# Kernel optimization log

Measured on AMD Instinct MI355X. Metric: run time of the kernel, lower is better.

Reference implementation:

```python
import jax, jax.numpy as jnp
import numpy as np


def _dwconv(x, w, pad):
    # depthwise conv, NCHW, weight (C,1,kh,kw), feature_group_count=C
    return jax.lax.conv_general_dilated(
        x, w, window_strides=(1, 1), padding=pad,
        feature_group_count=x.shape[1],
        dimension_numbers=('NCHW', 'OIHW', 'NCHW'))


def _max_channel_relu(x):
    # assumed MaxChannelReLU: keep only the channel-max value at each (b,h,w)
    return x * (x == jnp.max(x, axis=1, keepdims=True))


def setup_inputs() -> dict:
    key = jax.random.key(0)
    ks = jax.random.split(key, 6)
    B, C, H, W = 16, 64, 128, 128
    x = jax.random.normal(ks[0], (B, C, H, W), dtype=jnp.float32)
    w_bbx = 0.1 * jax.random.normal(ks[1], (C, 1, 1, 1), dtype=jnp.float32)
    w_width = 0.1 * jax.random.normal(ks[2], (C, 1, 1, 11), dtype=jnp.float32)
    w_width_sh = 0.1 * jax.random.normal(ks[3], (C, 1, 1, 1), dtype=jnp.float32)
    w_height = 0.1 * jax.random.normal(ks[4], (C, 1, 11, 1), dtype=jnp.float32)
    w_height_sh = 0.1 * jax.random.normal(ks[5], (C, 1, 1, 1), dtype=jnp.float32)
    return {"x": x, "w_bbx": w_bbx, "w_width": w_width,
            "w_width_sh": w_width_sh, "w_height": w_height,
            "w_height_sh": w_height_sh}


def reference(x, w_bbx, w_width, w_width_sh, w_height, w_height_sh):
    B, C, H, W = x.shape
    # self.bbx: depthwise 1x1 conv == per-channel scale
    wh = x * w_bbx.reshape(1, C, 1, 1)
    # width branch: depthwise (1,11) conv pad 5, scaled by W, then shared 1x1
    w = _dwconv(wh, w_width, [(0, 0), (5, 5)]) * W
    w = w * w_width_sh.reshape(1, C, 1, 1)
    # height branch: depthwise (11,1) conv pad 5, scaled by H, then shared 1x1
    h = _dwconv(wh, w_height, [(5, 5), (0, 0)]) * H
    h = h * w_height_sh.reshape(1, C, 1, 1)
    sx = jax.nn.sigmoid(x)
    M = jnp.max(sx, axis=(-2, -1), keepdims=True) - 0.01
    score = x * (sx > M).astype(x.dtype)
    S = jnp.sum(score, axis=(-2, -1), keepdims=True)
    sn = score / S  # normalized weights, reused by all weighted reductions
    ws = jnp.sum(w * sn, axis=(-2, -1))
    hs = jnp.sum(h * sn, axis=(-2, -1))
    ps = jnp.max(sx, axis=(-2, -1))
    col = jnp.arange(W, dtype=x.dtype).reshape(1, 1, 1, W)
    row = jnp.arange(H, dtype=x.dtype).reshape(1, 1, H, 1)
    x1 = jnp.sum(col * sn, axis=(-2, -1)) - ws / 2
    y1 = jnp.sum(row * sn, axis=(-2, -1)) - hs / 2
    x2 = x1 + ws
    y2 = y1 + hs
    score_m = _max_channel_relu(score)
    w_m = _max_channel_relu(w)
    h_m = _max_channel_relu(h)
    i = jnp.broadcast_to(jnp.arange(B, dtype=x.dtype)[:, None], (B, C))
    bbox = jnp.stack([i, x1, y1, x2, y2, ps], axis=-1).reshape(-1, 6)
    return jnp.concatenate([score_m, w_m, h_m], axis=1), bbox
```

## Files before the change

### kernel.cpp

```cpp
#include <hip/hip_runtime.h>
#include <math.h>

#define BATCH 16
#define CH    64
#define HH    128
#define WW    128
#define PLANE (HH*WW)
#define LROW  144
#define LROWS 138
#define OUT0  (BATCH*3*CH*PLANE)


__global__ __launch_bounds__(256) void k_max(const float* __restrict__ x,
                                             float* __restrict__ ws) {
    int bid = blockIdx.x;
    const float4* xp = (const float4*)(x + (size_t)bid * PLANE);
    int tid = threadIdx.x;
    float m = -INFINITY;
#pragma unroll
    for (int i = 0; i < 16; i++) {
        float4 v = xp[i * 256 + tid];
        m = fmaxf(m, fmaxf(fmaxf(v.x, v.y), fmaxf(v.z, v.w)));
    }
#pragma unroll
    for (int off = 32; off; off >>= 1) m = fmaxf(m, __shfl_xor(m, off, 64));
    __shared__ float sm[4];
    int wid = tid >> 6, lane = tid & 63;
    if (lane == 0) sm[wid] = m;
    __syncthreads();
    if (tid == 0) {
        float mm = fmaxf(fmaxf(sm[0], sm[1]), fmaxf(sm[2], sm[3]));
        float ps = 1.0f / (1.0f + expf(-mm));
        ws[bid] = ps - 0.01f;
        ws[1024 + bid] = ps;
    }
}

__global__ __launch_bounds__(256) void k_fields(
    const float* __restrict__ x,
    const float* __restrict__ w_bbx, const float* __restrict__ w_width,
    const float* __restrict__ w_width_sh, const float* __restrict__ w_height,
    const float* __restrict__ w_height_sh,
    float* __restrict__ ws, float* __restrict__ out) {
    __shared__ float xs[LROWS * LROW];
    __shared__ float red[4 * 5];
    int bid = blockIdx.x;
    int b = bid >> 6, c = bid & 63;
    int tid = threadIdx.x;

    for (int i = tid; i < LROWS * LROW; i += 256) xs[i] = 0.0f;
    __syncthreads();
    const float* xp = x + (size_t)bid * PLANE;
#pragma unroll
    for (int i = 0; i < 16; i++) {
        int idx = i * 256 + tid;
        int p = idx * 4;
        int y = p >> 7, xc = p & 127;
        float4 v = ((const float4*)xp)[idx];
        *(float4*)&xs[(y + 5) * LROW + xc + 8] = v;
    }
    float wk[11], hk[11];
#pragma unroll
    for (int k = 0; k < 11; k++) {
        wk[k] = w_width[c * 11 + k];
        hk[k] = w_height[c * 11 + k];
    }
    float cb = w_bbx[c];
    float cw = 128.0f * w_width_sh[c] * cb;
    float chs = 128.0f * w_height_sh[c] * cb;
    float M = ws[bid];
    __syncthreads();

    float S = 0.f, Sw = 0.f, Sh = 0.f, Scol = 0.f, Srow = 0.f;
    float* outS = out + (size_t)(b * 192 + c) * PLANE;
    float* outW = out + (size_t)(b * 192 + 64 + c) * PLANE;
    float* outH = out + (size_t)(b * 192 + 128 + c) * PLANE;

    for (int g = 0; g < 16; g++) {
        int idx = g * 256 + tid;
        int p = idx * 4;
        int y = p >> 7, xc = p & 127;
        float4 vx;
        float hx = 0.f, hy = 0.f, hz = 0.f, hw = 0.f;
#pragma unroll
        for (int k = 0; k < 11; k++) {
            float4 v = *(const float4*)&xs[(y + k) * LROW + xc + 8];
            if (k == 5) vx = v;
            hx += v.x * hk[k]; hy += v.y * hk[k];
            hz += v.z * hk[k]; hw += v.w * hk[k];
        }
        float wbuf[20];
        {
            float4 a0 = *(const float4*)&xs[(y + 5) * LROW + xc + 0];
            float4 a1 = *(const float4*)&xs[(y + 5) * LROW + xc + 4];
            float4 a3 = *(const float4*)&xs[(y + 5) * LROW + xc + 12];
            float4 a4 = *(const float4*)&xs[(y + 5) * LROW + xc + 16];
            wbuf[0] = a0.x;  wbuf[1] = a0.y;  wbuf[2] = a0.z;  wbuf[3] = a0.w;
            wbuf[4] = a1.x;  wbuf[5] = a1.y;  wbuf[6] = a1.z;  wbuf[7] = a1.w;
            wbuf[8] = vx.x;  wbuf[9] = vx.y;  wbuf[10] = vx.z; wbuf[11] = vx.w;
            wbuf[12] = a3.x; wbuf[13] = a3.y; wbuf[14] = a3.z; wbuf[15] = a3.w;
            wbuf[16] = a4.x; wbuf[17] = a4.y; wbuf[18] = a4.z; wbuf[19] = a4.w;
        }
        float wo[4];
#pragma unroll
        for (int j = 0; j < 4; j++) {
            float acc = 0.f;
#pragma unroll
            for (int k = 0; k < 11; k++) acc += wbuf[j + 3 + k] * wk[k];
            wo[j] = acc * cw;
        }
        float ho[4] = {hx * chs, hy * chs, hz * chs, hw * chs};
        float xv[4] = {vx.x, vx.y, vx.z, vx.w};
        float sc[4];
#pragma unroll
        for (int j = 0; j < 4; j++) {
            float sx = 1.0f / (1.0f + expf(-xv[j]));
            sc[j] = (sx > M) ? xv[j] : 0.0f;
        }
        float s4 = sc[0] + sc[1] + sc[2] + sc[3];
        S += s4;
        Srow += (float)y * s4;
#pragma unroll
        for (int j = 0; j < 4; j++) {
            Sw += wo[j] * sc[j];
            Sh += ho[j] * sc[j];
            Scol += (float)(xc + j) * sc[j];
        }
        float4 o;
        o.x = sc[0]; o.y = sc[1]; o.z = sc[2]; o.w = sc[3];
        ((float4*)outS)[idx] = o;
        o.x = wo[0]; o.y = wo[1]; o.z = wo[2]; o.w = wo[3];
        ((float4*)outW)[idx] = o;
        o.x = ho[0]; o.y = ho[1]; o.z = ho[2]; o.w = ho[3];
        ((float4*)outH)[idx] = o;
    }
#pragma unroll
    for (int off = 32; off; off >>= 1) {
        S    += __shfl_xor(S, off, 64);
        Sw   += __shfl_xor(Sw, off, 64);
        Sh   += __shfl_xor(Sh, off, 64);
        Scol += __shfl_xor(Scol, off, 64);
        Srow += __shfl_xor(Srow, off, 64);
    }
    int wid = tid >> 6, lane = tid & 63;
    if (lane == 0) {
        red[wid * 5 + 0] = S;   red[wid * 5 + 1] = Sw;
        red[wid * 5 + 2] = Sh;  red[wid * 5 + 3] = Scol;
        red[wid * 5 + 4] = Srow;
    }
    __syncthreads();
    if (tid == 0) {
        float a0 = 0, a1 = 0, a2 = 0, a3 = 0, a4 = 0;
#pragma unroll
        for (int w2 = 0; w2 < 4; w2++) {
            a0 += red[w2 * 5 + 0]; a1 += red[w2 * 5 + 1];
            a2 += red[w2 * 5 + 2]; a3 += red[w2 * 5 + 3];
            a4 += red[w2 * 5 + 4];
        }
        ws[2048 + bid] = a0;
        ws[3072 + bid] = a1;
        ws[4096 + bid] = a2;
        ws[5120 + bid] = a3;
        ws[6144 + bid] = a4;
    }
}

__global__ __launch_bounds__(256) void k_mask(float* __restrict__ out) {
    __shared__ float T[64 * 256];
    int bid = blockIdx.x;
    int b = bid >> 6;
    int p0 = (bid & 63) * 256;
    int tid = threadIdx.x;
    for (int f = 0; f < 3; f++) {
        size_t base = ((size_t)b * 192 + (size_t)f * 64) * PLANE + p0;
#pragma unroll
        for (int ci = 0; ci < 16; ci++) {
            int ch = ci * 4 + (tid >> 6);
            int px = (tid & 63) * 4;
            float4 v = *(const float4*)&out[base + (size_t)ch * PLANE + px];
            *(float4*)&T[ch * 256 + px] = v;
        }
        __syncthreads();
        float m = -INFINITY;
#pragma unroll
        for (int cc = 0; cc < 64; cc++) m = fmaxf(m, T[cc * 256 + tid]);
#pragma unroll
        for (int cc = 0; cc < 64; cc++) {
            float v = T[cc * 256 + tid];
            T[cc * 256 + tid] = (v == m) ? v : 0.0f;
        }
        __syncthreads();
#pragma unroll
        for (int ci = 0; ci < 16; ci++) {
            int ch = ci * 4 + (tid >> 6);
            int px = (tid & 63) * 4;
            float4 v = *(const float4*)&T[ch * 256 + px];
            *(float4*)&out[base + (size_t)ch * PLANE + px] = v;
        }
        __syncthreads();
    }
}

__global__ __launch_bounds__(256) void k_bbox(const float* __restrict__ ws,
                                              float* __restrict__ out) {
    int idx = blockIdx.x * 256 + threadIdx.x;
    if (idx >= 1024) return;
    int b = idx >> 6;
    float S    = ws[2048 + idx];
    float Sw   = ws[3072 + idx];
    float Sh   = ws[4096 + idx];
    float Scol = ws[5120 + idx];
    float Srow = ws[6144 + idx];
    float ps   = ws[1024 + idx];
    float inv = 1.0f / S;
    float wsv = Sw * inv, hsv = Sh * inv;
    float x1 = Scol * inv - 0.5f * wsv;
    float y1 = Srow * inv - 0.5f * hsv;
    float* o = out + OUT0 + (size_t)idx * 6;
    o[0] = (float)b;
    o[1] = x1;
    o[2] = y1;
    o[3] = x1 + wsv;
    o[4] = y1 + hsv;
    o[5] = ps;
}

extern "C" void kernel_launch(void* const* d_in, const int* in_sizes, int n_in,
                              void* d_out, int out_size, void* d_ws, size_t ws_size,
                              hipStream_t stream) {
    const float* x          = (const float*)d_in[0];
    const float* w_bbx      = (const float*)d_in[1];
    const float* w_width    = (const float*)d_in[2];
    const float* w_width_sh = (const float*)d_in[3];
    const float* w_height   = (const float*)d_in[4];
    const float* w_height_sh= (const float*)d_in[5];
    float* out = (float*)d_out;
    float* ws  = (float*)d_ws;

    k_max<<<dim3(1024), dim3(256), 0, stream>>>(x, ws);
    k_fields<<<dim3(1024), dim3(256), 0, stream>>>(
        x, w_bbx, w_width, w_width_sh, w_height, w_height_sh, ws, out);
    k_mask<<<dim3(1024), dim3(256), 0, stream>>>(out);
    k_bbox<<<dim3(4), dim3(256), 0, stream>>>(ws, out);
}
```

Before: 316.4 us.

## Precompute channel-max maps and fuse max-channel masking into field writer

Adds a pass that recomputes the width/height convolutions and score per pixel across all channels to build channel-max maps. The main kernel then applies the max-channel mask as it writes, eliminating the separate read-modify-write pass over the full output. The sigmoid threshold is also turned into an equivalent logit threshold on x, avoiding exp per element. The cost is redundant convolution compute and extra workspace for the max maps, and the k_cmax grid of only 256 blocks may underfill the GPU.

```diff
diff --git a/kernel.cpp b/kernel.cpp
--- a/kernel.cpp
+++ b/kernel.cpp
@@ -6,12 +6,65 @@
 #define HH    128
 #define WW    128
 #define PLANE (HH*WW)
+#define OUT0  (BATCH*3*CH*PLANE)
+
 #define LROW  144
 #define LROWS 138
-#define OUT0  (BATCH*3*CH*PLANE)
-
+
+#define CW_OFF  7168
+#define CHS_OFF 7232
+#define MW_OFF  8192
+#define MH_OFF  270336
+#define MS_OFF  532480
+
+__device__ __forceinline__ void conv4(const float* __restrict__ base,
+                                      const float* __restrict__ wk,
+                                      const float* __restrict__ hk,
+                                      float cw, float chs, float T,
+                                      float4& w4, float4& h4, float4& s4) {
+    float4 vx;
+    float hx = 0.f, hy = 0.f, hz = 0.f, hw = 0.f;
+#pragma unroll
+    for (int k = 0; k < 11; k++) {
+        float4 v = *(const float4*)(base + k * 144 + 8);
+        if (k == 5) vx = v;
+        hx = fmaf(v.x, hk[k], hx);
+        hy = fmaf(v.y, hk[k], hy);
+        hz = fmaf(v.z, hk[k], hz);
+        hw = fmaf(v.w, hk[k], hw);
+    }
+    float wbuf[20];
+    {
+        float4 a0 = *(const float4*)(base + 5 * 144 + 0);
+        float4 a1 = *(const float4*)(base + 5 * 144 + 4);
+        float4 a3 = *(const float4*)(base + 5 * 144 + 12);
+        float4 a4 = *(const float4*)(base + 5 * 144 + 16);
+        wbuf[0] = a0.x;  wbuf[1] = a0.y;  wbuf[2] = a0.z;  wbuf[3] = a0.w;
+        wbuf[4] = a1.x;  wbuf[5] = a1.y;  wbuf[6] = a1.z;  wbuf[7] = a1.w;
+        wbuf[8] = vx.x;  wbuf[9] = vx.y;  wbuf[10] = vx.z; wbuf[11] = vx.w;
+        wbuf[12] = a3.x; wbuf[13] = a3.y; wbuf[14] = a3.z; wbuf[15] = a3.w;
+        wbuf[16] = a4.x; wbuf[17] = a4.y; wbuf[18] = a4.z; wbuf[19] = a4.w;
+    }
+    float wo[4];
+#pragma unroll
+    for (int j = 0; j < 4; j++) {
+        float acc = 0.f;
+#pragma unroll
+        for (int k = 0; k < 11; k++) acc = fmaf(wbuf[j + 3 + k], wk[k], acc);
+        wo[j] = acc * cw;
+    }
+    w4.x = wo[0]; w4.y = wo[1]; w4.z = wo[2]; w4.w = wo[3];
+    h4.x = hx * chs; h4.y = hy * chs; h4.z = hz * chs; h4.w = hw * chs;
+    s4.x = (vx.x > T) ? vx.x : 0.f;
+    s4.y = (vx.y > T) ? vx.y : 0.f;
+    s4.z = (vx.z > T) ? vx.z : 0.f;
+    s4.w = (vx.w > T) ? vx.w : 0.f;
+}
 
 __global__ __launch_bounds__(256) void k_max(const float* __restrict__ x,
+                                             const float* __restrict__ w_bbx,
+                                             const float* __restrict__ w_width_sh,
+                                             const float* __restrict__ w_height_sh,
                                              float* __restrict__ ws) {
     int bid = blockIdx.x;
     const float4* xp = (const float4*)(x + (size_t)bid * PLANE);
@@ -31,16 +84,84 @@
     if (tid == 0) {
         float mm = fmaxf(fmaxf(sm[0], sm[1]), fmaxf(sm[2], sm[3]));
         float ps = 1.0f / (1.0f + expf(-mm));
-        ws[bid] = ps - 0.01f;
+        float M = ps - 0.01f;
+        float T = (M > 0.0f) ? logf(M / (1.0f - M)) : -INFINITY;
+        ws[bid] = T;
         ws[1024 + bid] = ps;
     }
-}
-
-__global__ __launch_bounds__(256) void k_fields(
+    if (bid < 64 && tid == 1) {
+        float cb = w_bbx[bid];
+        ws[CW_OFF + bid]  = 128.0f * w_width_sh[bid] * cb;
+        ws[CHS_OFF + bid] = 128.0f * w_height_sh[bid] * cb;
+    }
+}
+
+__global__ __launch_bounds__(256) void k_cmax(const float* __restrict__ x,
+                                              const float* __restrict__ w_width,
+                                              const float* __restrict__ w_height,
+                                              float* __restrict__ ws) {
+    __shared__ float4 xs4[4 * 18 * 36];
+    float* xs = (float*)xs4;
+    int bid = blockIdx.x;
+    int b = bid >> 4;
+    int r0 = (bid & 15) * 8;
+    int tid = threadIdx.x;
+
+    for (int i = tid; i < 4 * 18 * 36; i += 256)
+        xs4[i] = make_float4(0.f, 0.f, 0.f, 0.f);
+
+    int lr_o = tid >> 5;
+    int c0 = (tid & 31) << 2;
+
+    float4 mw = make_float4(-INFINITY, -INFINITY, -INFINITY, -INFINITY);
+    float4 mh = mw, ms = mw;
+
+    for (int ch0 = 0; ch0 < 64; ch0 += 4) {
+        __syncthreads();
+        for (int j = tid; j < 4 * 576; j += 256) {
+            int i = j / 576;
+            int rem = j - i * 576;
+            int lr = rem >> 5;
+            int c4 = rem & 31;
+            int gr = r0 - 5 + lr;
+            if (gr >= 0 && gr < 128) {
+                float4 v = *(const float4*)(x +
+                    ((size_t)((b * 64 + ch0 + i) * 128 + gr)) * 128 + c4 * 4);
+                *(float4*)(xs + (i * 18 + lr) * 144 + 8 + c4 * 4) = v;
+            }
+        }
+        __syncthreads();
+#pragma unroll
+        for (int i = 0; i < 4; i++) {
+            int c = ch0 + i;
+            float T   = ws[b * 64 + c];
+            float cw  = ws[CW_OFF + c];
+            float chs = ws[CHS_OFF + c];
+            float wk[11], hk[11];
+#pragma unroll
+            for (int k = 0; k < 11; k++) {
+                wk[k] = w_width[c * 11 + k];
+                hk[k] = w_height[c * 11 + k];
+            }
+            float4 w4, h4, s4;
+            conv4(xs + (i * 18 + lr_o) * 144 + c0, wk, hk, cw, chs, T, w4, h4, s4);
+            mw.x = fmaxf(mw.x, w4.x); mw.y = fmaxf(mw.y, w4.y);
+            mw.z = fmaxf(mw.z, w4.z); mw.w = fmaxf(mw.w, w4.w);
+            mh.x = fmaxf(mh.x, h4.x); mh.y = fmaxf(mh.y, h4.y);
+            mh.z = fmaxf(mh.z, h4.z); mh.w = fmaxf(mh.w, h4.w);
+            ms.x = fmaxf(ms.x, s4.x); ms.y = fmaxf(ms.y, s4.y);
+            ms.z = fmaxf(ms.z, s4.z); ms.w = fmaxf(ms.w, s4.w);
+        }
+    }
+    int p = b * PLANE + (r0 + lr_o) * 128 + c0;
+    *(float4*)(ws + MW_OFF + p) = mw;
+    *(float4*)(ws + MH_OFF + p) = mh;
+    *(float4*)(ws + MS_OFF + p) = ms;
+}
+
+__global__ __launch_bounds__(256) void k_write(
     const float* __restrict__ x,
-    const float* __restrict__ w_bbx, const float* __restrict__ w_width,
-    const float* __restrict__ w_width_sh, const float* __restrict__ w_height,
-    const float* __restrict__ w_height_sh,
+    const float* __restrict__ w_width, const float* __restrict__ w_height,
     float* __restrict__ ws, float* __restrict__ out) {
     __shared__ float xs[LROWS * LROW];
     __shared__ float red[4 * 5];
@@ -65,73 +186,56 @@
         wk[k] = w_width[c * 11 + k];
         hk[k] = w_height[c * 11 + k];
     }
-    float cb = w_bbx[c];
-    float cw = 128.0f * w_width_sh[c] * cb;
-    float chs = 128.0f * w_height_sh[c] * cb;
-    float M = ws[bid];
+    float T   = ws[bid];
+    float cw  = ws[CW_OFF + c];
+    float chs = ws[CHS_OFF + c];
     __syncthreads();
 
     float S = 0.f, Sw = 0.f, Sh = 0.f, Scol = 0.f, Srow = 0.f;
     float* outS = out + (size_t)(b * 192 + c) * PLANE;
     float* outW = out + (size_t)(b * 192 + 64 + c) * PLANE;
     float* outH = out + (size_t)(b * 192 + 128 + c) * PLANE;
+    const float* mwp = ws + MW_OFF + b * PLANE;
+    const float* mhp = ws + MH_OFF + b * PLANE;
+    const float* msp = ws + MS_OFF + b * PLANE;
 
     for (int g = 0; g < 16; g++) {
         int idx = g * 256 + tid;
         int p = idx * 4;
         int y = p >> 7, xc = p & 127;
-        float4 vx;
-        float hx = 0.f, hy = 0.f, hz = 0.f, hw = 0.f;
-#pragma unroll
-        for (int k = 0; k < 11; k++) {
-            float4 v = *(const float4*)&xs[(y + k) * LROW + xc + 8];
-            if (k == 5) vx = v;
-            hx += v.x * hk[k]; hy += v.y * hk[k];
-            hz += v.z * hk[k]; hw += v.w * hk[k];
-        }
-        float wbuf[20];
-        {
-            float4 a0 = *(const float4*)&xs[(y + 5) * LROW + xc + 0];
-            float4 a1 = *(const float4*)&xs[(y + 5) * LROW + xc + 4];
-            float4 a3 = *(const float4*)&xs[(y + 5) * LROW + xc + 12];
-            float4 a4 = *(const float4*)&xs[(y + 5) * LROW + xc + 16];
-            wbuf[0] = a0.x;  wbuf[1] = a0.y;  wbuf[2] = a0.z;  wbuf[3] = a0.w;
-            wbuf[4] = a1.x;  wbuf[5] = a1.y;  wbuf[6] = a1.z;  wbuf[7] = a1.w;
-            wbuf[8] = vx.x;  wbuf[9] = vx.y;  wbuf[10] = vx.z; wbuf[11] = vx.w;
-            wbuf[12] = a3.x; wbuf[13] = a3.y; wbuf[14] = a3.z; wbuf[15] = a3.w;
-            wbuf[16] = a4.x; wbuf[17] = a4.y; wbuf[18] = a4.z; wbuf[19] = a4.w;
-        }
-        float wo[4];
-#pragma unroll
-        for (int j = 0; j < 4; j++) {
-            float acc = 0.f;
-#pragma unroll
-            for (int k = 0; k < 11; k++) acc += wbuf[j + 3 + k] * wk[k];
-            wo[j] = acc * cw;
-        }
-        float ho[4] = {hx * chs, hy * chs, hz * chs, hw * chs};
-        float xv[4] = {vx.x, vx.y, vx.z, vx.w};
-        float sc[4];
-#pragma unroll
-        for (int j = 0; j < 4; j++) {
-            float sx = 1.0f / (1.0f + expf(-xv[j]));
-            sc[j] = (sx > M) ? xv[j] : 0.0f;
-        }
-        float s4 = sc[0] + sc[1] + sc[2] + sc[3];
-        S += s4;
-        Srow += (float)y * s4;
-#pragma unroll
-        for (int j = 0; j < 4; j++) {
-            Sw += wo[j] * sc[j];
-            Sh += ho[j] * sc[j];
-            Scol += (float)(xc + j) * sc[j];
-        }
+        float4 w4, h4, s4;
+        conv4(xs + y * LROW + xc, wk, hk, cw, chs, T, w4, h4, s4);
+
+        float s4sum = s4.x + s4.y + s4.z + s4.w;
+        S += s4sum;
+        Srow += (float)y * s4sum;
+        Sw = fmaf(w4.x, s4.x, Sw); Sw = fmaf(w4.y, s4.y, Sw);
+        Sw = fmaf(w4.z, s4.z, Sw); Sw = fmaf(w4.w, s4.w, Sw);
+        Sh = fmaf(h4.x, s4.x, Sh); Sh = fmaf(h4.y, s4.y, Sh);
+        Sh = fmaf(h4.z, s4.z, Sh); Sh = fmaf(h4.w, s4.w, Sh);
+        Scol = fmaf((float)(xc + 0), s4.x, Scol);
+        Scol = fmaf((float)(xc + 1), s4.y, Scol);
+        Scol = fmaf((float)(xc + 2), s4.z, Scol);
+        Scol = fmaf((float)(xc + 3), s4.w, Scol);
+
+        float4 mw = *(const float4*)(mwp + p);
+        float4 mh = *(const float4*)(mhp + p);
+        float4 ms = *(const float4*)(msp + p);
         float4 o;
-        o.x = sc[0]; o.y = sc[1]; o.z = sc[2]; o.w = sc[3];
+        o.x = (s4.x == ms.x) ? s4.x : 0.f;
+        o.y = (s4.y == ms.y) ? s4.y : 0.f;
+        o.z = (s4.z == ms.z) ? s4.z : 0.f;
+        o.w = (s4.w == ms.w) ? s4.w : 0.f;
         ((float4*)outS)[idx] = o;
-        o.x = wo[0]; o.y = wo[1]; o.z = wo[2]; o.w = wo[3];
+        o.x = (w4.x == mw.x) ? w4.x : 0.f;
+        o.y = (w4.y == mw.y) ? w4.y : 0.f;
+        o.z = (w4.z == mw.z) ? w4.z : 0.f;
+        o.w = (w4.w == mw.w) ? w4.w : 0.f;
         ((float4*)outW)[idx] = o;
-        o.x = ho[0]; o.y = ho[1]; o.z = ho[2]; o.w = ho[3];
+        o.x = (h4.x == mh.x) ? h4.x : 0.f;
+        o.y = (h4.y == mh.y) ? h4.y : 0.f;
+        o.z = (h4.z == mh.z) ? h4.z : 0.f;
+        o.w = (h4.w == mh.w) ? h4.w : 0.f;
         ((float4*)outH)[idx] = o;
     }
 #pragma unroll
@@ -162,42 +266,6 @@
         ws[4096 + bid] = a2;
         ws[5120 + bid] = a3;
         ws[6144 + bid] = a4;
-    }
-}
-
-__global__ __launch_bounds__(256) void k_mask(float* __restrict__ out) {
-    __shared__ float T[64 * 256];
-    int bid = blockIdx.x;
-    int b = bid >> 6;
-    int p0 = (bid & 63) * 256;
-    int tid = threadIdx.x;
-    for (int f = 0; f < 3; f++) {
-        size_t base = ((size_t)b * 192 + (size_t)f * 64) * PLANE + p0;
-#pragma unroll
-        for (int ci = 0; ci < 16; ci++) {
-            int ch = ci * 4 + (tid >> 6);
-            int px = (tid & 63) * 4;
-            float4 v = *(const float4*)&out[base + (size_t)ch * PLANE + px];
-            *(float4*)&T[ch * 256 + px] = v;
-        }
-        __syncthreads();
-        float m = -INFINITY;
-#pragma unroll
-        for (int cc = 0; cc < 64; cc++) m = fmaxf(m, T[cc * 256 + tid]);
-#pragma unroll
-        for (int cc = 0; cc < 64; cc++) {
-            float v = T[cc * 256 + tid];
-            T[cc * 256 + tid] = (v == m) ? v : 0.0f;
-        }
-        __syncthreads();
-#pragma unroll
-        for (int ci = 0; ci < 16; ci++) {
-            int ch = ci * 4 + (tid >> 6);
-            int px = (tid & 63) * 4;
-            float4 v = *(const float4*)&T[ch * 256 + px];
-            *(float4*)&out[base + (size_t)ch * PLANE + px] = v;
-        }
-        __syncthreads();
     }
 }
 
@@ -237,9 +305,8 @@
     float* out = (float*)d_out;
     float* ws  = (float*)d_ws;
 
-    k_max<<<dim3(1024), dim3(256), 0, stream>>>(x, ws);
-    k_fields<<<dim3(1024), dim3(256), 0, stream>>>(
-        x, w_bbx, w_width, w_width_sh, w_height, w_height_sh, ws, out);
-    k_mask<<<dim3(1024), dim3(256), 0, stream>>>(out);
+    k_max<<<dim3(1024), dim3(256), 0, stream>>>(x, w_bbx, w_width_sh, w_height_sh, ws);
+    k_cmax<<<dim3(256), dim3(256), 0, stream>>>(x, w_width, w_height, ws);
+    k_write<<<dim3(1024), dim3(256), 0, stream>>>(x, w_width, w_height, ws, out);
     k_bbox<<<dim3(4), dim3(256), 0, stream>>>(ws, out);
 }
```

Measured after the change: 356.2 us. +12.6%, slower.
